# Kernel tuning notes

Measured on AMD Instinct MI355X. Metric: run time of the kernel, lower is better.

## Reference

```python
import jax, jax.numpy as jnp
import numpy as np

EPS = 1e-12


def _pchip_slopes(knots, y):
    # knots: (K,), y: (..., K) -> slopes (..., K), faithful to torch _pchip_slopes
    h = knots[1:] - knots[:-1]                       # (K-1,)
    delta = (y[..., 1:] - y[..., :-1]) / (h + EPS)   # (..., K-1)
    h0, h1 = h[:-1], h[1:]
    w1 = 2 * h1 + h0
    w2 = h1 + 2 * h0
    del0 = delta[..., :-1]
    del1 = delta[..., 1:]
    same_sign = del0 * del1 > 0
    d_int = (w1 + w2) / (w1 / (del0 + EPS) + w2 / (del1 + EPS) + EPS)
    d_mid = jnp.where(same_sign, d_int, jnp.zeros_like(d_int))
    # left endpoint (one-sided, shape-preserving)
    d0 = ((2 * h[0] + h[1]) * delta[..., 0] - h[0] * delta[..., 1]) / (h[0] + h[1] + EPS)
    d0 = jnp.where(d0 * delta[..., 0] <= 0, jnp.zeros_like(d0), d0)
    d0 = jnp.where((delta[..., 0] * delta[..., 1] < 0) & (jnp.abs(d0) > 3 * jnp.abs(delta[..., 0])),
                   3 * delta[..., 0], d0)
    # right endpoint
    dn = ((2 * h[-1] + h[-2]) * delta[..., -1] - h[-1] * delta[..., -2]) / (h[-1] + h[-2] + EPS)
    dn = jnp.where(dn * delta[..., -1] <= 0, jnp.zeros_like(dn), dn)
    dn = jnp.where((delta[..., -1] * delta[..., -2] < 0) & (jnp.abs(dn) > 3 * jnp.abs(delta[..., -1])),
                   3 * delta[..., -1], dn)
    return jnp.concatenate([d0[..., None], d_mid, dn[..., None]], axis=-1)


def _kan_forward(x, knots, coeffs, bias):
    d_out, d_in, K = coeffs.shape
    slopes = _pchip_slopes(knots, coeffs)            # (d_out, d_in, K)
    x0, xN = knots[0], knots[-1]
    dx = (xN - x0) / (K - 1)
    u = (x - x0) / (dx + EPS)                        # (B, d_in)
    idx = jnp.clip(jnp.floor(u).astype(jnp.int32), 0, K - 2)  # (B, d_in)
    t = u - idx.astype(u.dtype)                      # (B, d_in)

    # Gather knot values/slopes per batch row without materializing (B,d_out,d_in,K)
    def gather_row(i, ip1):
        def g(tbl, ii):
            ii_b = jnp.broadcast_to(ii[None, :, None], (d_out, d_in, 1))
            return jnp.take_along_axis(tbl, ii_b, axis=-1)[..., 0]
        return g(coeffs, i), g(coeffs, ip1), g(slopes, i), g(slopes, ip1)

    yk, yk1, mk, mk1 = jax.vmap(gather_row)(idx, idx + 1)  # each (B, d_out, d_in)

    t2 = t * t
    t3 = t2 * t
    h00 = (2 * t3 - 3 * t2 + 1)[:, None, :]
    h10 = (t3 - 2 * t2 + t)[:, None, :]
    h01 = (-2 * t3 + 3 * t2)[:, None, :]
    h11 = (t3 - t2)[:, None, :]
    y_mid = h00 * yk + h10 * dx * mk + h01 * yk1 + h11 * dx * mk1  # (B, d_out, d_in)

    mask_left = (x < x0)[:, None, :]
    mask_right = (x > xN)[:, None, :]
    mask_mid = ~mask_left & ~mask_right
    y_left = coeffs[None, ..., 0] + slopes[None, ..., 0] * (x - x0)[:, None, :]
    y_right = coeffs[None, ..., -1] + slopes[None, ..., -1] * (x - xN)[:, None, :]

    y = jnp.where(mask_mid, y_mid, jnp.zeros_like(y_mid))
    y = jnp.where(mask_left, y_left, y)
    y = jnp.where(mask_right, y_right, y)
    return y.sum(axis=-1) + bias                     # (B, d_out)


def setup_inputs() -> dict:
    key = jax.random.key(0)
    k1, k2 = jax.random.split(key)
    B, d_in, d_out, K = 256, 512, 512, 16
    # sample slightly outside [0,1] to exercise linear extrapolation branches
    x = jax.random.uniform(k1, (B, d_in), dtype=jnp.float32, minval=-0.1, maxval=1.1)
    knots = jnp.linspace(0.0, 1.0, K, dtype=jnp.float32)
    std = 0.02 / np.sqrt(d_in)
    coeffs = jax.random.normal(k2, (d_out, d_in, K), dtype=jnp.float32) * std
    bias = jnp.zeros((d_out,), dtype=jnp.float32)
    return {"x": x, "knots": knots, "coeffs": coeffs, "bias": bias}


def reference(x, knots, coeffs, bias):
    return _kan_forward(x, knots, coeffs, bias)
```

## Files before the change

kernel.cpp:

```cpp
#include <hip/hip_runtime.h>

#define EPSF 1e-12f

#define B_SZ 256
#define DIN 512
#define DOUT 512
#define KN 16
#define NSEG 15

#define O_TILE 32
#define I_CHUNK 16
#define N_CHUNK (DIN / I_CHUNK)
#define ROW_W 34
#define ROW_B (ROW_W * 4)

__global__ __launch_bounds__(256) void kan_weights(
    const float* __restrict__ x, const float* __restrict__ knots,
    float4* __restrict__ w4, int* __restrict__ koff) {
  int flat = blockIdx.x * 256 + threadIdx.x;
  int b = flat & (B_SZ - 1);
  int i = flat >> 8;
  float x0 = knots[0];
  float xN = knots[KN - 1];
  float dx = (xN - x0) / (float)(KN - 1);
  float xv = x[b * DIN + i];
  float4 w;
  int k;
  if (xv < x0) {
    w = make_float4(1.f, xv - x0, 0.f, 0.f); k = 0;
  } else if (xv > xN) {
    w = make_float4(0.f, 0.f, 1.f, xv - xN); k = NSEG - 1;
  } else {
    float u = (xv - x0) / (dx + EPSF);
    k = (int)floorf(u);
    if (k > NSEG - 1) k = NSEG - 1;
    float t = u - (float)k;
    float t2 = t * t, t3 = t2 * t;
    w = make_float4(2.f * t3 - 3.f * t2 + 1.f,
                    dx * (t3 - 2.f * t2 + t),
                    -2.f * t3 + 3.f * t2,
                    dx * (t3 - t2));
  }
  w4[i * B_SZ + b] = w;
  koff[i * B_SZ + b] = k * 8;
}

__global__ __launch_bounds__(256) void kan_main(
    const float* __restrict__ coeffs, const float* __restrict__ knots,
    const float4* __restrict__ w4, const int* __restrict__ koff,
    float* __restrict__ part) {
  __shared__ float tbl[O_TILE * I_CHUNK * ROW_W];
  int bid = blockIdx.x;
  int c  = bid >> 4;
  int ot = bid & 15;
  int i0 = c * I_CHUNK;
  int o0 = ot * O_TILE;
  int t = threadIdx.x;

  float kn[KN];
#pragma unroll
  for (int j = 0; j < 4; ++j) {
    float4 kk = reinterpret_cast<const float4*>(knots)[j];
    kn[4 * j + 0] = kk.x; kn[4 * j + 1] = kk.y;
    kn[4 * j + 2] = kk.z; kn[4 * j + 3] = kk.w;
  }
  float h[NSEG];
#pragma unroll
  for (int j = 0; j < NSEG; ++j) h[j] = kn[j + 1] - kn[j];

#pragma unroll
  for (int rep = 0; rep < 2; ++rep) {
    int r  = t + rep * 256;
    int il = r & 15;
    int ol = r >> 4;
    const float* crow = coeffs + ((size_t)(o0 + ol) * DIN + (i0 + il)) * KN;
    float C[KN];
#pragma unroll
    for (int j = 0; j < 4; ++j) {
      float4 v = reinterpret_cast<const float4*>(crow)[j];
      C[4 * j + 0] = v.x; C[4 * j + 1] = v.y;
      C[4 * j + 2] = v.z; C[4 * j + 3] = v.w;
    }
    float del[NSEG];
#pragma unroll
    for (int j = 0; j < NSEG; ++j) del[j] = (C[j + 1] - C[j]) / (h[j] + EPSF);
    float d[KN];
    {
      float d0 = ((2.f * h[0] + h[1]) * del[0] - h[0] * del[1]) / (h[0] + h[1] + EPSF);
      if (d0 * del[0] <= 0.f) d0 = 0.f;
      else if (del[0] * del[1] < 0.f && fabsf(d0) > 3.f * fabsf(del[0])) d0 = 3.f * del[0];
      d[0] = d0;
      float dn = ((2.f * h[14] + h[13]) * del[14] - h[14] * del[13]) / (h[14] + h[13] + EPSF);
      if (dn * del[14] <= 0.f) dn = 0.f;
      else if (del[14] * del[13] < 0.f && fabsf(dn) > 3.f * fabsf(del[14])) dn = 3.f * del[14];
      d[15] = dn;
    }
#pragma unroll
    for (int j = 1; j <= 14; ++j) {
      float del0 = del[j - 1], del1 = del[j];
      float w1 = 2.f * h[j] + h[j - 1];
      float w2 = h[j] + 2.f * h[j - 1];
      float e0 = del0 + EPSF, e1 = del1 + EPSF;
      float prod = e0 * e1;
      float dj = (w1 + w2) * prod / (w1 * e1 + w2 * e0 + EPSF * prod);
      d[j] = (del0 * del1 > 0.f) ? dj : 0.f;
    }
    float2* rowp = reinterpret_cast<float2*>(&tbl[r * ROW_W]);
#pragma unroll
    for (int j = 0; j < KN; ++j) rowp[j] = make_float2(C[j], d[j]);
  }
  __syncthreads();

  float acc[O_TILE];
#pragma unroll
  for (int o = 0; o < O_TILE; ++o) acc[o] = 0.f;
  int b = t;
  for (int il = 0; il < I_CHUNK; ++il) {
    float4 w = w4[(i0 + il) * B_SZ + b];
    int kb = koff[(i0 + il) * B_SZ + b];
    const char* base = reinterpret_cast<const char*>(tbl) + il * ROW_B + kb;
#pragma unroll
    for (int ol = 0; ol < O_TILE; ++ol) {
      float2 p0 = *reinterpret_cast<const float2*>(base + ol * (I_CHUNK * ROW_B));
      float2 p1 = *reinterpret_cast<const float2*>(base + ol * (I_CHUNK * ROW_B) + 8);
      acc[ol] = fmaf(w.x, p0.x,
                fmaf(w.y, p0.y,
                fmaf(w.z, p1.x,
                fmaf(w.w, p1.y, acc[ol]))));
    }
  }
#pragma unroll
  for (int ol = 0; ol < O_TILE; ++ol)
    part[((size_t)c * DOUT + (o0 + ol)) * B_SZ + b] = acc[ol];
}

__global__ __launch_bounds__(256) void kan_reduce(
    const float* __restrict__ part, const float* __restrict__ bias,
    float* __restrict__ out) {
  int flat = blockIdx.x * 256 + threadIdx.x;
  int b = flat & (B_SZ - 1);
  int o = flat >> 8;
  float acc = bias[o];
#pragma unroll 4
  for (int c = 0; c < N_CHUNK; ++c)
    acc += part[((size_t)c * DOUT + o) * B_SZ + b];
  out[b * DOUT + o] = acc;
}

extern "C" void kernel_launch(void* const* d_in, const int* in_sizes, int n_in,
                              void* d_out, int out_size, void* d_ws, size_t ws_size,
                              hipStream_t stream) {
  const float* x      = (const float*)d_in[0];
  const float* knots  = (const float*)d_in[1];
  const float* coeffs = (const float*)d_in[2];
  const float* bias   = (const float*)d_in[3];
  float* out = (float*)d_out;

  char* ws = (char*)d_ws;
  float*  part = (float*)ws;
  float4* w4   = (float4*)(ws + (size_t)16 * 1024 * 1024);
  int*    koff = (int*)(ws + (size_t)18 * 1024 * 1024);

  kan_weights<<<512, 256, 0, stream>>>(x, knots, w4, koff);
  kan_main   <<<512, 256, 0, stream>>>(coeffs, knots, w4, koff, part);
  kan_reduce <<<512, 256, 0, stream>>>(part, bias, out);
}
```

Before: 104.4 us.

## Fuse weight computation into main kernel, pack table in fp16, vectorize reduce

The separate Hermite-weight kernel is removed and the weights are computed inline from x inside the main kernel. The shared-memory spline table now stores coefficient/slope pairs for each segment as packed fp16 in uint2 slots, so each output needs a single 8-byte LDS read. The reduce kernel is vectorized with float4 loads over the batch, and launch bounds now request 2 blocks per SM. Storing the table in fp16 loses precision relative to the fp32 reference, and the inline x reads are strided per thread.

```diff
diff --git a/kernel.cpp b/kernel.cpp
--- a/kernel.cpp
+++ b/kernel.cpp
@@ -11,45 +11,20 @@
 #define O_TILE 32
 #define I_CHUNK 16
 #define N_CHUNK (DIN / I_CHUNK)
-#define ROW_W 34
-#define ROW_B (ROW_W * 4)
 
-__global__ __launch_bounds__(256) void kan_weights(
-    const float* __restrict__ x, const float* __restrict__ knots,
-    float4* __restrict__ w4, int* __restrict__ koff) {
-  int flat = blockIdx.x * 256 + threadIdx.x;
-  int b = flat & (B_SZ - 1);
-  int i = flat >> 8;
-  float x0 = knots[0];
-  float xN = knots[KN - 1];
-  float dx = (xN - x0) / (float)(KN - 1);
-  float xv = x[b * DIN + i];
-  float4 w;
-  int k;
-  if (xv < x0) {
-    w = make_float4(1.f, xv - x0, 0.f, 0.f); k = 0;
-  } else if (xv > xN) {
-    w = make_float4(0.f, 0.f, 1.f, xv - xN); k = NSEG - 1;
-  } else {
-    float u = (xv - x0) / (dx + EPSF);
-    k = (int)floorf(u);
-    if (k > NSEG - 1) k = NSEG - 1;
-    float t = u - (float)k;
-    float t2 = t * t, t3 = t2 * t;
-    w = make_float4(2.f * t3 - 3.f * t2 + 1.f,
-                    dx * (t3 - 2.f * t2 + t),
-                    -2.f * t3 + 3.f * t2,
-                    dx * (t3 - t2));
-  }
-  w4[i * B_SZ + b] = w;
-  koff[i * B_SZ + b] = k * 8;
+#define ROW_SLOTS 17
+
+union H2U { _Float16 h[2]; unsigned u; };
+__device__ __forceinline__ unsigned packh2(float a, float b) {
+  H2U v; v.h[0] = (_Float16)a; v.h[1] = (_Float16)b; return v.u;
 }
+__device__ __forceinline__ float loh(unsigned u) { H2U v; v.u = u; return (float)v.h[0]; }
+__device__ __forceinline__ float hih(unsigned u) { H2U v; v.u = u; return (float)v.h[1]; }
 
-__global__ __launch_bounds__(256) void kan_main(
-    const float* __restrict__ coeffs, const float* __restrict__ knots,
-    const float4* __restrict__ w4, const int* __restrict__ koff,
-    float* __restrict__ part) {
-  __shared__ float tbl[O_TILE * I_CHUNK * ROW_W];
+__global__ __launch_bounds__(256, 2) void kan_main(
+    const float* __restrict__ x, const float* __restrict__ coeffs,
+    const float* __restrict__ knots, float* __restrict__ part) {
+  __shared__ uint2 tbl[O_TILE * I_CHUNK * ROW_SLOTS];
   int bid = blockIdx.x;
   int c  = bid >> 4;
   int ot = bid & 15;
@@ -67,6 +42,8 @@
   float h[NSEG];
 #pragma unroll
   for (int j = 0; j < NSEG; ++j) h[j] = kn[j + 1] - kn[j];
+  float x0 = kn[0], xN = kn[KN - 1];
+  float dx = (xN - x0) / (float)(KN - 1);
 
 #pragma unroll
   for (int rep = 0; rep < 2; ++rep) {
@@ -105,9 +82,10 @@
       float dj = (w1 + w2) * prod / (w1 * e1 + w2 * e0 + EPSF * prod);
       d[j] = (del0 * del1 > 0.f) ? dj : 0.f;
     }
-    float2* rowp = reinterpret_cast<float2*>(&tbl[r * ROW_W]);
+    uint2* rowp = &tbl[r * ROW_SLOTS];
 #pragma unroll
-    for (int j = 0; j < KN; ++j) rowp[j] = make_float2(C[j], d[j]);
+    for (int k = 0; k < NSEG; ++k)
+      rowp[k] = make_uint2(packh2(C[k], d[k]), packh2(C[k + 1], d[k + 1]));
   }
   __syncthreads();
 
@@ -115,18 +93,35 @@
 #pragma unroll
   for (int o = 0; o < O_TILE; ++o) acc[o] = 0.f;
   int b = t;
+  const float* xrow = x + (size_t)b * DIN + i0;
+#pragma unroll
   for (int il = 0; il < I_CHUNK; ++il) {
-    float4 w = w4[(i0 + il) * B_SZ + b];
-    int kb = koff[(i0 + il) * B_SZ + b];
-    const char* base = reinterpret_cast<const char*>(tbl) + il * ROW_B + kb;
+    float xv = xrow[il];
+    float wx, wy, wz, ww;
+    int kk;
+    if (xv < x0) {
+      wx = 1.f; wy = xv - x0; wz = 0.f; ww = 0.f; kk = 0;
+    } else if (xv > xN) {
+      wx = 0.f; wy = 0.f; wz = 1.f; ww = xv - xN; kk = NSEG - 1;
+    } else {
+      float u = (xv - x0) / (dx + EPSF);
+      kk = (int)u;
+      if (kk > NSEG - 1) kk = NSEG - 1;
+      float tt = u - (float)kk;
+      float t2 = tt * tt, t3 = t2 * tt;
+      wx = 2.f * t3 - 3.f * t2 + 1.f;
+      wy = dx * (t3 - 2.f * t2 + tt);
+      wz = -2.f * t3 + 3.f * t2;
+      ww = dx * (t3 - t2);
+    }
+    const uint2* bp = &tbl[il * ROW_SLOTS + kk];
 #pragma unroll
     for (int ol = 0; ol < O_TILE; ++ol) {
-      float2 p0 = *reinterpret_cast<const float2*>(base + ol * (I_CHUNK * ROW_B));
-      float2 p1 = *reinterpret_cast<const float2*>(base + ol * (I_CHUNK * ROW_B) + 8);
-      acc[ol] = fmaf(w.x, p0.x,
-                fmaf(w.y, p0.y,
-                fmaf(w.z, p1.x,
-                fmaf(w.w, p1.y, acc[ol]))));
+      uint2 q = bp[ol * (ROW_SLOTS * I_CHUNK)];
+      acc[ol] = fmaf(wx, loh(q.x),
+                fmaf(wy, hih(q.x),
+                fmaf(wz, loh(q.y),
+                fmaf(ww, hih(q.y), acc[ol]))));
     }
   }
 #pragma unroll
@@ -135,16 +130,23 @@
 }
 
 __global__ __launch_bounds__(256) void kan_reduce(
-    const float* __restrict__ part, const float* __restrict__ bias,
+    const float4* __restrict__ part4, const float* __restrict__ bias,
     float* __restrict__ out) {
   int flat = blockIdx.x * 256 + threadIdx.x;
-  int b = flat & (B_SZ - 1);
-  int o = flat >> 8;
-  float acc = bias[o];
-#pragma unroll 4
-  for (int c = 0; c < N_CHUNK; ++c)
-    acc += part[((size_t)c * DOUT + o) * B_SZ + b];
-  out[b * DOUT + o] = acc;
+  int bg = flat & 63;
+  int o  = flat >> 6;
+  float4 a = make_float4(0.f, 0.f, 0.f, 0.f);
+#pragma unroll 8
+  for (int c = 0; c < N_CHUNK; ++c) {
+    float4 p = part4[((size_t)c * DOUT + o) * (B_SZ / 4) + bg];
+    a.x += p.x; a.y += p.y; a.z += p.z; a.w += p.w;
+  }
+  float bb = bias[o];
+  int b0 = bg * 4;
+  out[(size_t)(b0 + 0) * DOUT + o] = a.x + bb;
+  out[(size_t)(b0 + 1) * DOUT + o] = a.y + bb;
+  out[(size_t)(b0 + 2) * DOUT + o] = a.z + bb;
+  out[(size_t)(b0 + 3) * DOUT + o] = a.w + bb;
 }
 
 extern "C" void kernel_launch(void* const* d_in, const int* in_sizes, int n_in,
@@ -156,12 +158,8 @@
   const float* bias   = (const float*)d_in[3];
   float* out = (float*)d_out;
 
-  char* ws = (char*)d_ws;
-  float*  part = (float*)ws;
-  float4* w4   = (float4*)(ws + (size_t)16 * 1024 * 1024);
-  int*    koff = (int*)(ws + (size_t)18 * 1024 * 1024);
+  float* part = (float*)d_ws;
 
-  kan_weights<<<512, 256, 0, stream>>>(x, knots, w4, koff);
-  kan_main   <<<512, 256, 0, stream>>>(coeffs, knots, w4, koff, part);
-  kan_reduce <<<512, 256, 0, stream>>>(part, bias, out);
+  kan_main  <<<512, 256, 0, stream>>>(x, coeffs, knots, part);
+  kan_reduce<<<128, 256, 0, stream>>>((const float4*)part, bias, out);
 }
```

New measurement: 385.8 us. 270% more time.
